# Kernel tuning notes

Hardware: AMD Instinct MI355X
Metric: run time of the kernel (lower is better)

## Reference

```python
import jax, jax.numpy as jnp
import numpy as np

N_NODES = 50000
N_EDGES = 800000
F_IN = 128
HIDDEN = 96
N_CLASS = 40


def setup_inputs() -> dict:
    key = jax.random.key(0)
    ks = jax.random.split(key, 16)
    x = jax.random.normal(ks[0], (N_NODES, F_IN), dtype=jnp.float32)
    edge_index = jax.random.randint(ks[1], (2, N_EDGES), 0, N_NODES, dtype=jnp.int64)
    edge_weight = jax.random.uniform(ks[2], (N_EDGES,), dtype=jnp.float32)
    s = 0.1
    return {
        "x": x,
        "edge_index": edge_index,
        "edge_weight": edge_weight,
        "W_conv1": jax.random.normal(ks[3], (F_IN, HIDDEN), dtype=jnp.float32) * s,
        "b_conv1": jnp.zeros((HIDDEN,), dtype=jnp.float32),
        "W_conv2": jax.random.normal(ks[4], (HIDDEN, HIDDEN), dtype=jnp.float32) * s,
        "b_conv2": jnp.zeros((HIDDEN,), dtype=jnp.float32),
        "W_conv3": jax.random.normal(ks[5], (HIDDEN, HIDDEN), dtype=jnp.float32) * s,
        "b_conv3": jnp.zeros((HIDDEN,), dtype=jnp.float32),
        "W_lin1": jax.random.normal(ks[6], (F_IN, HIDDEN), dtype=jnp.float32) * s,
        "b_lin1": jnp.zeros((HIDDEN,), dtype=jnp.float32),
        "W_lin2": jax.random.normal(ks[7], (HIDDEN, N_CLASS), dtype=jnp.float32) * s,
        "b_lin2": jnp.zeros((N_CLASS,), dtype=jnp.float32),
    }


def _gcn_norm(edge_index, edge_weight, num_nodes):
    # PyG gcn_norm: add self-loops (weight 1), symmetric deg^-1/2 normalization.
    row, col = edge_index[0], edge_index[1]
    loop = jnp.arange(num_nodes, dtype=edge_index.dtype)
    rows = jnp.concatenate([row, loop])
    cols = jnp.concatenate([col, loop])
    w = jnp.concatenate([edge_weight, jnp.ones((num_nodes,), edge_weight.dtype)])
    deg = jax.ops.segment_sum(w, cols, num_segments=num_nodes)
    dinv = jnp.where(deg > 0, jax.lax.rsqrt(deg), 0.0)
    norm = dinv[rows] * w * dinv[cols]  # [E + N]
    return rows, cols, norm


def _gcn_conv(x, rows, cols, norm, W, b, num_nodes):
    h = x @ W                                   # [N, H]
    msg = norm[:, None] * h[rows]               # gather + scale, [E+N, H]
    out = jax.ops.segment_sum(msg, cols, num_segments=num_nodes)  # scatter-add
    return out + b


def reference(x, edge_index, edge_weight, W_conv1, b_conv1, W_conv2, b_conv2,
              W_conv3, b_conv3, W_lin1, b_lin1, W_lin2, b_lin2):
    N = x.shape[0]
    rows, cols, norm = _gcn_norm(edge_index, edge_weight, N)
    # x1 = elu(conv1(x)); residual branch through first_lin + stacked convs
    x1 = jax.nn.elu(_gcn_conv(x, rows, cols, norm, W_conv1, b_conv1, N))
    h = jax.nn.elu(x @ W_lin1 + b_lin1)
    # dropout p=0.5 is identity in eval mode
    h = jax.nn.elu(_gcn_conv(h, rows, cols, norm, W_conv2, b_conv2, N))
    h = jax.nn.elu(_gcn_conv(h, rows, cols, norm, W_conv3, b_conv3, N))
    h = x1 + h
    logits = h @ W_lin2 + b_lin2
    return jax.nn.log_softmax(logits, axis=-1)
```

## Files before the change

### kernel.cpp

```cpp
#include <hip/hip_runtime.h>
#include <hip/hip_bf16.h>

static __device__ __forceinline__ float elu_f(float x) {
    return x > 0.f ? x : expm1f(x);
}

static __device__ __forceinline__ ushort f2bf(float x) {
    __hip_bfloat16 h = __float2bfloat16(x);
    ushort u;
    __builtin_memcpy(&u, &h, 2);
    return u;
}

typedef short bf16x8 __attribute__((ext_vector_type(8)));
typedef float f32x4  __attribute__((ext_vector_type(4)));
typedef float floatx2 __attribute__((ext_vector_type(2)));

#if __has_builtin(__builtin_amdgcn_cvt_pk_f32_fp8) && __has_builtin(__builtin_amdgcn_cvt_pk_fp8_f32)
#define FP8_HW 1
#else
#define FP8_HW 0
#endif

static __device__ __forceinline__ float fp8_to_f32_sw(uint b) {
    uint s = (b & 0x80u) << 24;
    uint e = (b >> 3) & 0xfu, m = b & 7u;
    float v = (e == 0) ? ((float)m * 0x1p-9f)
                       : __uint_as_float(((e + 120u) << 23) | (m << 20));
    return __uint_as_float(s | __float_as_uint(v));
}

static __device__ __forceinline__ uint f32_to_fp8_sw(float x) {
    float c = fminf(fmaxf(x, -448.f), 448.f);
    uint s = (__float_as_uint(c) >> 24) & 0x80u;
    float a = fabsf(c);
    uint bits;
    if (a < 0x1p-6f) {
        int mi = (int)rintf(a * 0x1p9f);
        bits = (mi >= 8) ? 0x08u : (uint)mi;
    } else {
        uint u = __float_as_uint(a);
        int eb = (int)((u >> 23) & 0xff) - 127;
        float sc = a * exp2f((float)(3 - eb));
        int q = (int)rintf(sc);
        if (q >= 16) { q = 8; eb += 1; }
        bits = (eb > 8) ? 0x7eu : (((uint)(eb + 7) << 3) | (uint)(q - 8));
    }
    return s | bits;
}

static __device__ __forceinline__ uchar f2fp8(float v) {
#if FP8_HW
    return (uchar)((uint)__builtin_amdgcn_cvt_pk_fp8_f32(v, v, 0, false) & 0xffu);
#else
    return (uchar)f32_to_fp8_sw(v);
#endif
}

static __device__ __forceinline__ void fp8x4_unpack(uint w, float* f) {
#if FP8_HW
    floatx2 p0 = __builtin_amdgcn_cvt_pk_f32_fp8((int)w, false);
    floatx2 p1 = __builtin_amdgcn_cvt_pk_f32_fp8((int)w, true);
    f[0] = p0[0]; f[1] = p0[1]; f[2] = p1[0]; f[3] = p1[1];
#else
    f[0] = fp8_to_f32_sw(w & 0xffu);
    f[1] = fp8_to_f32_sw((w >> 8) & 0xffu);
    f[2] = fp8_to_f32_sw((w >> 16) & 0xffu);
    f[3] = fp8_to_f32_sw(w >> 24);
#endif
}

static __device__ __forceinline__ void fp8x16_unpack(uint4 v, float* f) {
    fp8x4_unpack(v.x, f);
    fp8x4_unpack(v.y, f + 4);
    fp8x4_unpack(v.z, f + 8);
    fp8x4_unpack(v.w, f + 12);
}

static __device__ __forceinline__ void bf8_unpack(uint4 v, float* f) {
    f[0] = __uint_as_float(v.x << 16);
    f[1] = __uint_as_float(v.x & 0xffff0000u);
    f[2] = __uint_as_float(v.y << 16);
    f[3] = __uint_as_float(v.y & 0xffff0000u);
    f[4] = __uint_as_float(v.z << 16);
    f[5] = __uint_as_float(v.z & 0xffff0000u);
    f[6] = __uint_as_float(v.w << 16);
    f[7] = __uint_as_float(v.w & 0xffff0000u);
}

static __device__ __forceinline__ uint4 bf8_pack(const float* a) {
    uint4 o;
    o.x = (uint)f2bf(a[0]) | ((uint)f2bf(a[1]) << 16);
    o.y = (uint)f2bf(a[2]) | ((uint)f2bf(a[3]) << 16);
    o.z = (uint)f2bf(a[4]) | ((uint)f2bf(a[5]) << 16);
    o.w = (uint)f2bf(a[6]) | ((uint)f2bf(a[7]) << 16);
    return o;
}

__global__ __launch_bounds__(256) void
k_wprep_count(const float* __restrict__ W1, const float* __restrict__ W2,
              const float* __restrict__ W3, const float* __restrict__ W4,
              ushort* __restrict__ T1, ushort* __restrict__ T2,
              ushort* __restrict__ T3, ushort* __restrict__ T4,
              const int* __restrict__ col, int* __restrict__ bcnt,
              int E, int bspan, int nW) {
    const int b = blockIdx.x;
    if (b < nW) {
        const float* W; ushort* T; int K, base;
        if      (b < 48)  { W = W1; T = T1; K = 128; base = b;       }
        else if (b < 96)  { W = W2; T = T2; K = 128; base = b - 48;  }
        else if (b < 132) { W = W3; T = T3; K = 96;  base = b - 96;  }
        else              { W = W4; T = T4; K = 96;  base = b - 132; }
        const int i = base * 256 + threadIdx.x;
        const int kk = i / 96, c = i - kk * 96;
        T[c * K + kk] = f2bf(W[i]);
    } else {
        __shared__ int h[256];
        const int tid = threadIdx.x;
        h[tid] = 0;
        __syncthreads();
        const int e0 = (b - nW) * 4096;
        #pragma unroll
        for (int j = 0; j < 16; ++j) {
            int e = e0 + j * 256 + tid;
            if (e < E) atomicAdd(&h[col[e] / bspan], 1);
        }
        __syncthreads();
        if (h[tid] > 0) atomicAdd(&bcnt[tid], h[tid]);
    }
}

__global__ __launch_bounds__(256) void
k_bscatter(const int* __restrict__ row, const int* __restrict__ col,
           const float* __restrict__ w, const int* __restrict__ bcnt,
           int* __restrict__ bRes, int2* __restrict__ ebuf, int* __restrict__ edst,
           int E, int bspan) {
    __shared__ int h[256];
    __shared__ int base[256];
    __shared__ int sOff[256];
    __shared__ int wsum[4];
    const int tid = threadIdx.x, lane = tid & 63, wid = tid >> 6;
    h[tid] = 0;
    const int bc = bcnt[tid];
    __syncthreads();
    const int e0 = blockIdx.x * 4096;
    int bk[16], rk[16];
    #pragma unroll
    for (int j = 0; j < 16; ++j) {
        int e = e0 + j * 256 + tid;
        if (e < E) {
            int b = col[e] / bspan;
            bk[j] = b;
            rk[j] = atomicAdd(&h[b], 1);
        }
    }
    {
        int s = bc;
        #pragma unroll
        for (int d = 1; d < 64; d <<= 1) {
            int t = __shfl_up(s, d);
            if (lane >= d) s += t;
        }
        if (lane == 63) wsum[wid] = s;
        __syncthreads();
        int wb = 0;
        #pragma unroll
        for (int k = 0; k < 3; ++k) if (k < wid) wb += wsum[k];
        sOff[tid] = s - bc + wb;
    }
    __syncthreads();
    base[tid] = (h[tid] > 0) ? (sOff[tid] + atomicAdd(&bRes[tid], h[tid])) : 0;
    __syncthreads();
    #pragma unroll
    for (int j = 0; j < 16; ++j) {
        int e = e0 + j * 256 + tid;
        if (e < E) {
            int pos = base[bk[j]] + rk[j];
            ebuf[pos] = make_int2(row[e], __float_as_int(w[e]));
            edst[pos] = col[e];
        }
    }
}

__global__ __launch_bounds__(256) void
k_csrify(const int2* __restrict__ ebuf, const int* __restrict__ edst,
         const int* __restrict__ bcnt, int* __restrict__ off, float* __restrict__ dinv,
         int2* __restrict__ pairs, int N, int E, int bspan) {
    __shared__ int hist[256];
    __shared__ float degs[256];
    __shared__ int curl[256];
    __shared__ int wsum[4];
    __shared__ int sE0;
    const int tid = threadIdx.x, b = blockIdx.x;
    const int lane = tid & 63, wid = tid >> 6;
    const int base = b * bspan;
    const int lnodes = (N - base < bspan) ? (N - base) : bspan;
    if (b == 0 && tid == 0) off[N] = E;
    if (lnodes <= 0) return;
    hist[tid] = 0;
    degs[tid] = 0.f;
    const int bc = bcnt[tid];
    {
        int s = bc;
        #pragma unroll
        for (int d = 1; d < 64; d <<= 1) {
            int t = __shfl_up(s, d);
            if (lane >= d) s += t;
        }
        if (lane == 63) wsum[wid] = s;
        __syncthreads();
        int wb = 0;
        #pragma unroll
        for (int k = 0; k < 3; ++k) if (k < wid) wb += wsum[k];
        if (tid == b) sE0 = s - bc + wb;
    }
    __syncthreads();
    const int e0 = sE0, e1 = sE0 + bcnt[b];
    for (int e = e0 + tid; e < e1; e += 256) {
        int d = edst[e] - base;
        atomicAdd(&hist[d], 1);
        atomicAdd(&degs[d], __int_as_float(ebuf[e].y));
    }
    __syncthreads();
    int v = hist[tid];
    int s = v;
    #pragma unroll
    for (int d = 1; d < 64; d <<= 1) {
        int t = __shfl_up(s, d);
        if (lane >= d) s += t;
    }
    if (lane == 63) wsum[wid] = s;
    __syncthreads();
    int wb = 0;
    #pragma unroll
    for (int k = 0; k < 3; ++k) if (k < wid) wb += wsum[k];
    int excl = s - v + wb;
    if (tid < lnodes) {
        off[base + tid] = e0 + excl;
        dinv[base + tid] = rsqrtf(1.0f + degs[tid]);
    }
    curl[tid] = excl;
    __syncthreads();
    for (int e = e0 + tid; e < e1; e += 256) {
        int d = edst[e] - base;
        int p = atomicAdd(&curl[d], 1);
        pairs[e0 + p] = ebuf[e];
    }
}

template<int K, int XBF>
__device__ __forceinline__ void gemm_body(
    const void* __restrict__ Xv, const ushort* __restrict__ Wt,
    const float* __restrict__ bias, const float* __restrict__ dscale,
    void* __restrict__ outp, int N, int act, int ofp8, int bid) {
    constexpr int KP = K + 8;
    __shared__ ushort XT[64 * KP];
    __shared__ ushort WT[96 * KP];
    const int tid = threadIdx.x;
    const int n0  = bid * 64;

    #pragma unroll
    for (int i = tid; i < 96 * K / 8; i += 256) {
        const int c = i / (K / 8), q = i - c * (K / 8);
        uint4 v = reinterpret_cast<const uint4*>(Wt)[i];
        *reinterpret_cast<uint4*>(&WT[c * KP + q * 8]) = v;
    }
    if (XBF) {
        const ushort* X = (const ushort*)Xv;
        #pragma unroll
        for (int i = tid; i < 64 * K / 8; i += 256) {
            const int row = i / (K / 8), q = i - row * (K / 8);
            const int n = (n0 + row < N) ? (n0 + row) : (N - 1);
            uint4 v = *reinterpret_cast<const uint4*>(X + (size_t)n * K + q * 8);
            *reinterpret_cast<uint4*>(&XT[row * KP + q * 8]) = v;
        }
    } else {
        const float* X = (const float*)Xv;
        #pragma unroll
        for (int i = tid; i < 64 * K / 4; i += 256) {
            const int row = i / (K / 4), q = i - row * (K / 4);
            const int n = (n0 + row < N) ? (n0 + row) : (N - 1);
            float4 v = *reinterpret_cast<const float4*>(X + (size_t)n * K + q * 4);
            uint lo = (uint)f2bf(v.x) | ((uint)f2bf(v.y) << 16);
            uint hi = (uint)f2bf(v.z) | ((uint)f2bf(v.w) << 16);
            *reinterpret_cast<uint2*>(&XT[row * KP + q * 4]) = make_uint2(lo, hi);
        }
    }
    __syncthreads();

    const int lane = tid & 63;
    const int wv   = tid >> 6;
    const int r16  = lane & 15;
    const int kh   = lane >> 4;

    bf16x8 a[K / 32];
    const ushort* xbase = &XT[(wv * 16 + r16) * KP + kh * 8];
    #pragma unroll
    for (int ks = 0; ks < K / 32; ++ks)
        a[ks] = *reinterpret_cast<const bf16x8*>(xbase + ks * 32);

    f32x4 acc[6];
    #pragma unroll
    for (int ct = 0; ct < 6; ++ct) {
        f32x4 c = {0.f, 0.f, 0.f, 0.f};
        const ushort* wbase = &WT[(ct * 16 + r16) * KP + kh * 8];
        #pragma unroll
        for (int ks = 0; ks < K / 32; ++ks) {
            bf16x8 bfr = *reinterpret_cast<const bf16x8*>(wbase + ks * 32);
            c = __builtin_amdgcn_mfma_f32_16x16x32_bf16(a[ks], bfr, c, 0, 0, 0);
        }
        acc[ct] = c;
    }

    #pragma unroll
    for (int r = 0; r < 4; ++r) {
        const int n = n0 + wv * 16 + kh * 4 + r;
        if (n >= N) continue;
        const float ds = dscale ? dscale[n] : 1.f;
        #pragma unroll
        for (int ct = 0; ct < 6; ++ct) {
            const int col = ct * 16 + r16;
            float v = acc[ct][r] * ds;
            if (bias) v += bias[col];
            if (act) v = elu_f(v);
            if (ofp8) ((uchar*)outp)[(size_t)n * 96 + col] = f2fp8(v);
            else      ((ushort*)outp)[(size_t)n * 96 + col] = f2bf(v);
        }
    }
}

__global__ __launch_bounds__(256) void
k_gemm_mfma96(const ushort* __restrict__ X, const ushort* __restrict__ Wt,
              const float* __restrict__ dscale, void* __restrict__ outp, int N) {
    gemm_body<96, 1>(X, Wt, nullptr, dscale, outp, N, 0, 1, blockIdx.x);
}

__global__ __launch_bounds__(256) void
k_gemm_fin_dual(const float* __restrict__ X,
                const ushort* __restrict__ Wt1, const float* __restrict__ dscale1,
                void* __restrict__ out1,
                const ushort* __restrict__ Wt2, const float* __restrict__ bias2,
                void* __restrict__ out2, int N, int nHalf) {
    if ((int)blockIdx.x < nHalf)
        gemm_body<128, 0>(X, Wt1, nullptr, dscale1, out1, N, 0, 1, blockIdx.x);
    else
        gemm_body<128, 0>(X, Wt2, bias2, nullptr, out2, N, 1, 0, blockIdx.x - nHalf);
}

#define AGG_CAP 2048

__global__ __launch_bounds__(256) void
k_aggregate(const uchar* __restrict__ tmp, const int* __restrict__ off,
            const int2* __restrict__ pairs, const float* __restrict__ dinv,
            const float* __restrict__ bias, const ushort* __restrict__ addsrc,
            ushort* __restrict__ out, int N) {
    __shared__ int2 eP[AGG_CAP];
    __shared__ int sFlag;
    const int tid = threadIdx.x;
    const int t0  = blockIdx.x * 256;
    int n_first = t0 / 6;
    if (n_first >= N) return;
    int n_last = (t0 + 255) / 6;
    if (n_last >= N) n_last = N - 1;
    const int eb0 = off[n_first];
    const int eb1 = off[n_last + 1];
    const int tot = eb1 - eb0;
    if (tot <= AGG_CAP) {
        for (int i = tid; i < tot; i += 256) eP[i] = pairs[eb0 + i];
        if (tid == 0) sFlag = 1;
    } else if (tid == 0) sFlag = 0;
    __syncthreads();
    const bool lds = (sFlag != 0);

    const int n = (t0 + tid) / 6;
    if (n >= N) return;
    const int c = ((t0 + tid) % 6) * 16;
    const uchar* base = tmp + c;

    auto LOADP = [&](int e) -> int2 { return lds ? eP[e - eb0] : pairs[e]; };

    const float di = dinv[n];
    float f[16], acc[16];
    {
        uint4 sv = *reinterpret_cast<const uint4*>(base + (size_t)n * 96);
        fp8x16_unpack(sv, f);
        #pragma unroll
        for (int i = 0; i < 16; ++i) acc[i] = f[i];
    }

    const int e0 = off[n];
    const int e1 = off[n + 1];
    const int m  = e1 - e0;

    int2 pA, pB, pC;
    uint4 hA, hB, hC;
    if (m > 0) { pA = LOADP(e0);     hA = *reinterpret_cast<const uint4*>(base + (size_t)pA.x * 96); }
    if (m > 1) { pB = LOADP(e0 + 1); hB = *reinterpret_cast<const uint4*>(base + (size_t)pB.x * 96); }
    if (m > 2) { pC = LOADP(e0 + 2); hC = *reinterpret_cast<const uint4*>(base + (size_t)pC.x * 96); }

    for (int e = e0 + 3; e < e1; ++e) {
        int2 pD = LOADP(e);
        uint4 hD = *reinterpret_cast<const uint4*>(base + (size_t)pD.x * 96);
        float w = __int_as_float(pA.y);
        fp8x16_unpack(hA, f);
        #pragma unroll
        for (int i = 0; i < 16; ++i) acc[i] = fmaf(w, f[i], acc[i]);
        pA = pB; hA = hB;
        pB = pC; hB = hC;
        pC = pD; hC = hD;
    }
    if (m > 0) {
        float w = __int_as_float(pA.y);
        fp8x16_unpack(hA, f);
        #pragma unroll
        for (int i = 0; i < 16; ++i) acc[i] = fmaf(w, f[i], acc[i]);
    }
    if (m > 1) {
        float w = __int_as_float(pB.y);
        fp8x16_unpack(hB, f);
        #pragma unroll
        for (int i = 0; i < 16; ++i) acc[i] = fmaf(w, f[i], acc[i]);
    }
    if (m > 2) {
        float w = __int_as_float(pC.y);
        fp8x16_unpack(hC, f);
        #pragma unroll
        for (int i = 0; i < 16; ++i) acc[i] = fmaf(w, f[i], acc[i]);
    }

    #pragma unroll
    for (int q = 0; q < 4; ++q) {
        float4 bv = *reinterpret_cast<const float4*>(bias + c + q * 4);
        acc[q * 4 + 0] = elu_f(fmaf(di, acc[q * 4 + 0], bv.x));
        acc[q * 4 + 1] = elu_f(fmaf(di, acc[q * 4 + 1], bv.y));
        acc[q * 4 + 2] = elu_f(fmaf(di, acc[q * 4 + 2], bv.z));
        acc[q * 4 + 3] = elu_f(fmaf(di, acc[q * 4 + 3], bv.w));
    }
    if (addsrc) {
        uint4 r0 = *reinterpret_cast<const uint4*>(addsrc + (size_t)n * 96 + c);
        uint4 r1 = *reinterpret_cast<const uint4*>(addsrc + (size_t)n * 96 + c + 8);
        bf8_unpack(r0, f);
        bf8_unpack(r1, f + 8);
        #pragma unroll
        for (int i = 0; i < 16; ++i) acc[i] += f[i];
    }
    ushort* op = out + (size_t)n * 96 + c;
    *reinterpret_cast<uint4*>(op)     = bf8_pack(acc);
    *reinterpret_cast<uint4*>(op + 8) = bf8_pack(acc + 8);
}

__global__ __launch_bounds__(128) void
k_lin2_lsm(const ushort* __restrict__ h, const float* __restrict__ W2,
           const float* __restrict__ b2, float* __restrict__ out, int N) {
    __shared__ float hsT[96][128];
    const int tid = threadIdx.x;
    const int n0 = blockIdx.x * 128;
    const int nn = (N - n0 < 128) ? (N - n0) : 128;

    if (tid < nn) {
        const ushort* hr = h + (size_t)(n0 + tid) * 96;
        #pragma unroll
        for (int q = 0; q < 12; ++q) {
            uint4 v = *reinterpret_cast<const uint4*>(hr + q * 8);
            float f[8];
            bf8_unpack(v, f);
            #pragma unroll
            for (int j = 0; j < 8; ++j) hsT[q * 8 + j][tid] = f[j];
        }
    }
    __syncthreads();

    float acc[40];
    #pragma unroll
    for (int c = 0; c < 40; ++c) acc[c] = b2[c];
    for (int k = 0; k < 96; ++k) {
        const float hv = hsT[k][tid];
        const float* wr = W2 + k * 40;
        #pragma unroll
        for (int c = 0; c < 40; ++c) acc[c] = fmaf(hv, wr[c], acc[c]);
    }

    float m = acc[0];
    #pragma unroll
    for (int c = 1; c < 40; ++c) m = fmaxf(m, acc[c]);
    float s = 0.f;
    #pragma unroll
    for (int c = 0; c < 40; ++c) s += expf(acc[c] - m);
    const float lse = m + logf(s);

    if (tid < nn) {
        float* op = out + (size_t)(n0 + tid) * 40;
        #pragma unroll
        for (int q = 0; q < 10; ++q) {
            float4 v = make_float4(acc[q * 4 + 0] - lse, acc[q * 4 + 1] - lse,
                                   acc[q * 4 + 2] - lse, acc[q * 4 + 3] - lse);
            *reinterpret_cast<float4*>(op + q * 4) = v;
        }
    }
}


extern "C" void kernel_launch(void* const* d_in, const int* in_sizes, int n_in,
                              void* d_out, int out_size, void* d_ws, size_t ws_size,
                              hipStream_t stream) {
    const float* x   = (const float*)d_in[0];
    const int*   ei  = (const int*)d_in[1];
    const float* ew  = (const float*)d_in[2];
    const float* Wc1 = (const float*)d_in[3];
    const float* bc1 = (const float*)d_in[4];
    const float* Wc2 = (const float*)d_in[5];
    const float* bc2 = (const float*)d_in[6];
    const float* Wc3 = (const float*)d_in[7];
    const float* bc3 = (const float*)d_in[8];
    const float* Wl1 = (const float*)d_in[9];
    const float* bl1 = (const float*)d_in[10];
    const float* Wl2 = (const float*)d_in[11];
    const float* bl2 = (const float*)d_in[12];

    const int FIN = 128, HID = 96;
    const int N = in_sizes[0] / FIN;
    const int E = in_sizes[2];
    const int* row = ei;
    const int* col = ei + E;
    const int bspan = (N + 255) / 256;

    char* ws = (char*)d_ws;
    size_t o = 0;
    auto alloc = [&](size_t bytes) -> void* {
        void* p = ws + o;
        o += (bytes + 255) & ~(size_t)255;
        return p;
    };
    float*  dinv   = (float*)alloc((size_t)N * 4);
    int*    off    = (int*)  alloc((size_t)(N + 1) * 4);
    int*    bmem   = (int*)  alloc(512 * 4);
    int*    bcnt   = bmem;
    int*    bRes   = bmem + 256;
    int2*   pairs  = (int2*) alloc((size_t)E * 8);
    uchar*  M1     = (uchar*)alloc((size_t)N * HID);
    uchar*  M2     = (uchar*)alloc((size_t)N * HID);
    ushort* Bb     = (ushort*)alloc((size_t)N * HID * 2);
    ushort* Cb     = (ushort*)alloc((size_t)N * HID * 2);
    ushort* Wt_c1  = (ushort*)alloc(96 * 128 * 2);
    ushort* Wt_l1  = (ushort*)alloc(96 * 128 * 2);
    ushort* Wt_c2  = (ushort*)alloc(96 * 96 * 2);
    ushort* Wt_c3  = (ushort*)alloc(96 * 96 * 2);
    int2*   ebuf   = (int2*) alloc((size_t)E * 8);
    int*    edst   = (int*)  alloc((size_t)E * 4);

    const int gBkt  = (E + 4095) / 4096;
    const int nGemm = (N + 63) / 64;
    const int nAgg  = (N * 6 + 255) / 256;

    hipMemsetAsync(bmem, 0, 512 * 4, stream);
    k_wprep_count<<<168 + gBkt, 256, 0, stream>>>(Wc1, Wl1, Wc2, Wc3,
                                                  Wt_c1, Wt_l1, Wt_c2, Wt_c3,
                                                  col, bcnt, E, bspan, 168);

    k_bscatter<<<gBkt, 256, 0, stream>>>(row, col, ew, bcnt, bRes, ebuf, edst, E, bspan);
    k_csrify<<<256, 256, 0, stream>>>(ebuf, edst, bcnt, off, dinv, pairs, N, E, bspan);

    k_gemm_fin_dual<<<2 * nGemm, 256, 0, stream>>>(x, Wt_c1, dinv, M1,
                                                   Wt_l1, bl1, Cb, N, nGemm);

    k_aggregate<<<nAgg, 256, 0, stream>>>(M1, off, pairs, dinv, bc1, nullptr, Bb, N);

    k_gemm_mfma96<<<nGemm, 256, 0, stream>>>(Cb, Wt_c2, dinv, M2, N);
    k_aggregate<<<nAgg, 256, 0, stream>>>(M2, off, pairs, dinv, bc2, nullptr, Cb, N);

    k_gemm_mfma96<<<nGemm, 256, 0, stream>>>(Cb, Wt_c3, dinv, M1, N);
    k_aggregate<<<nAgg, 256, 0, stream>>>(M1, off, pairs, dinv, bc3, Bb, Cb, N);

    k_lin2_lsm<<<(N + 127) / 128, 128, 0, stream>>>(Cb, Wl2, bl2, (float*)d_out, N);
}
```

Baseline: 186.0 us.

## Fuse aggregation with next-layer GEMM and co-schedule independent stages

Runs the first aggregation and the conv2 GEMM in one launch, since the two are independent and can be split by block index. Fuses the second aggregation with the conv3 GEMM so aggregated rows stay in LDS as bf16 and feed MFMA directly, which avoids writing and re-reading the intermediate buffer. Also stores bf16 instead of float in the lin2 shared buffer to halve LDS use. This saves two launches and one global round trip, at the cost of a larger block with more LDS and lower occupancy in the fused kernel.

```diff
diff --git a/kernel.cpp b/kernel.cpp
--- a/kernel.cpp
+++ b/kernel.cpp
@@ -330,12 +330,6 @@
 }
 
 __global__ __launch_bounds__(256) void
-k_gemm_mfma96(const ushort* __restrict__ X, const ushort* __restrict__ Wt,
-              const float* __restrict__ dscale, void* __restrict__ outp, int N) {
-    gemm_body<96, 1>(X, Wt, nullptr, dscale, outp, N, 0, 1, blockIdx.x);
-}
-
-__global__ __launch_bounds__(256) void
 k_gemm_fin_dual(const float* __restrict__ X,
                 const ushort* __restrict__ Wt1, const float* __restrict__ dscale1,
                 void* __restrict__ out1,
@@ -349,15 +343,15 @@
 
 #define AGG_CAP 2048
 
-__global__ __launch_bounds__(256) void
-k_aggregate(const uchar* __restrict__ tmp, const int* __restrict__ off,
-            const int2* __restrict__ pairs, const float* __restrict__ dinv,
-            const float* __restrict__ bias, const ushort* __restrict__ addsrc,
-            ushort* __restrict__ out, int N) {
+__device__ __forceinline__ void agg_body(
+    const uchar* __restrict__ tmp, const int* __restrict__ off,
+    const int2* __restrict__ pairs, const float* __restrict__ dinv,
+    const float* __restrict__ bias, const ushort* __restrict__ addsrc,
+    ushort* __restrict__ out, int N, int bid) {
     __shared__ int2 eP[AGG_CAP];
     __shared__ int sFlag;
     const int tid = threadIdx.x;
-    const int t0  = blockIdx.x * 256;
+    const int t0  = bid * 256;
     int n_first = t0 / 6;
     if (n_first >= N) return;
     int n_last = (t0 + 255) / 6;
@@ -449,10 +443,160 @@
     *reinterpret_cast<uint4*>(op + 8) = bf8_pack(acc + 8);
 }
 
+__global__ __launch_bounds__(256) void
+k_aggregate(const uchar* __restrict__ tmp, const int* __restrict__ off,
+            const int2* __restrict__ pairs, const float* __restrict__ dinv,
+            const float* __restrict__ bias, const ushort* __restrict__ addsrc,
+            ushort* __restrict__ out, int N) {
+    agg_body(tmp, off, pairs, dinv, bias, addsrc, out, N, blockIdx.x);
+}
+
+__global__ __launch_bounds__(256) void
+k_agg1_gemm2(const uchar* __restrict__ M1, const int* __restrict__ off,
+             const int2* __restrict__ pairs, const float* __restrict__ dinv,
+             const float* __restrict__ bc1, ushort* __restrict__ Bb,
+             const ushort* __restrict__ Cb, const ushort* __restrict__ Wt2,
+             uchar* __restrict__ M2, int N, int nAgg) {
+    if ((int)blockIdx.x < nAgg)
+        agg_body(M1, off, pairs, dinv, bc1, nullptr, Bb, N, blockIdx.x);
+    else
+        gemm_body<96, 1>(Cb, Wt2, nullptr, dinv, M2, N, 0, 1, (int)blockIdx.x - nAgg);
+}
+
+#define FKP 104
+
+__global__ __launch_bounds__(384) void
+k_agg2_gemm3(const uchar* __restrict__ M2, const int* __restrict__ off,
+             const int2* __restrict__ pairs, const float* __restrict__ dinv,
+             const float* __restrict__ bc2, const ushort* __restrict__ Wt3,
+             uchar* __restrict__ M3, int N) {
+    __shared__ ushort XT[64 * FKP];
+    __shared__ ushort WT[96 * FKP];
+    __shared__ int2 eP[AGG_CAP];
+    __shared__ int sFlag;
+    const int tid = threadIdx.x;
+    const int n0  = blockIdx.x * 64;
+
+    for (int i = tid; i < 96 * 96 / 8; i += 384) {
+        const int c = i / 12, q = i - c * 12;
+        uint4 v = reinterpret_cast<const uint4*>(Wt3)[i];
+        *reinterpret_cast<uint4*>(&WT[c * FKP + q * 8]) = v;
+    }
+    int n_last = (n0 + 63 < N) ? (n0 + 63) : (N - 1);
+    const int eb0 = off[n0];
+    const int eb1 = off[n_last + 1];
+    const int tot = eb1 - eb0;
+    if (tot <= AGG_CAP) {
+        for (int i = tid; i < tot; i += 384) eP[i] = pairs[eb0 + i];
+        if (tid == 0) sFlag = 1;
+    } else if (tid == 0) sFlag = 0;
+    __syncthreads();
+    const bool lds = (sFlag != 0);
+
+    const int n = n0 + tid / 6;
+    const int c = (tid % 6) * 16;
+    float acc[16];
+    if (n < N) {
+        const uchar* base = M2 + c;
+        auto LOADP = [&](int e) -> int2 { return lds ? eP[e - eb0] : pairs[e]; };
+        float f[16];
+        {
+            uint4 sv = *reinterpret_cast<const uint4*>(base + (size_t)n * 96);
+            fp8x16_unpack(sv, f);
+            #pragma unroll
+            for (int i = 0; i < 16; ++i) acc[i] = f[i];
+        }
+        const int e0 = off[n];
+        const int e1 = off[n + 1];
+        const int m  = e1 - e0;
+        int2 pA, pB, pC;
+        uint4 hA, hB, hC;
+        if (m > 0) { pA = LOADP(e0);     hA = *reinterpret_cast<const uint4*>(base + (size_t)pA.x * 96); }
+        if (m > 1) { pB = LOADP(e0 + 1); hB = *reinterpret_cast<const uint4*>(base + (size_t)pB.x * 96); }
+        if (m > 2) { pC = LOADP(e0 + 2); hC = *reinterpret_cast<const uint4*>(base + (size_t)pC.x * 96); }
+        for (int e = e0 + 3; e < e1; ++e) {
+            int2 pD = LOADP(e);
+            uint4 hD = *reinterpret_cast<const uint4*>(base + (size_t)pD.x * 96);
+            float w = __int_as_float(pA.y);
+            fp8x16_unpack(hA, f);
+            #pragma unroll
+            for (int i = 0; i < 16; ++i) acc[i] = fmaf(w, f[i], acc[i]);
+            pA = pB; hA = hB;
+            pB = pC; hB = hC;
+            pC = pD; hC = hD;
+        }
+        if (m > 0) {
+            float w = __int_as_float(pA.y);
+            fp8x16_unpack(hA, f);
+            #pragma unroll
+            for (int i = 0; i < 16; ++i) acc[i] = fmaf(w, f[i], acc[i]);
+        }
+        if (m > 1) {
+            float w = __int_as_float(pB.y);
+            fp8x16_unpack(hB, f);
+            #pragma unroll
+            for (int i = 0; i < 16; ++i) acc[i] = fmaf(w, f[i], acc[i]);
+        }
+        if (m > 2) {
+            float w = __int_as_float(pC.y);
+            fp8x16_unpack(hC, f);
+            #pragma unroll
+            for (int i = 0; i < 16; ++i) acc[i] = fmaf(w, f[i], acc[i]);
+        }
+        const float di = dinv[n];
+        #pragma unroll
+        for (int q = 0; q < 4; ++q) {
+            float4 bv = *reinterpret_cast<const float4*>(bc2 + c + q * 4);
+            acc[q * 4 + 0] = elu_f(fmaf(di, acc[q * 4 + 0], bv.x));
+            acc[q * 4 + 1] = elu_f(fmaf(di, acc[q * 4 + 1], bv.y));
+            acc[q * 4 + 2] = elu_f(fmaf(di, acc[q * 4 + 2], bv.z));
+            acc[q * 4 + 3] = elu_f(fmaf(di, acc[q * 4 + 3], bv.w));
+        }
+    } else {
+        #pragma unroll
+        for (int i = 0; i < 16; ++i) acc[i] = 0.f;
+    }
+    {
+        ushort* xp = &XT[(tid / 6) * FKP + c];
+        *reinterpret_cast<uint4*>(xp)     = bf8_pack(acc);
+        *reinterpret_cast<uint4*>(xp + 8) = bf8_pack(acc + 8);
+    }
+    __syncthreads();
+
+    const int lane = tid & 63;
+    const int ct   = tid >> 6;
+    const int r16  = lane & 15;
+    const int kh   = lane >> 4;
+
+    bf16x8 b[3];
+    const ushort* wbase = &WT[(ct * 16 + r16) * FKP + kh * 8];
+    #pragma unroll
+    for (int ks = 0; ks < 3; ++ks)
+        b[ks] = *reinterpret_cast<const bf16x8*>(wbase + ks * 32);
+
+    #pragma unroll
+    for (int rt = 0; rt < 4; ++rt) {
+        f32x4 d = {0.f, 0.f, 0.f, 0.f};
+        const ushort* xb = &XT[(rt * 16 + r16) * FKP + kh * 8];
+        #pragma unroll
+        for (int ks = 0; ks < 3; ++ks) {
+            bf16x8 a = *reinterpret_cast<const bf16x8*>(xb + ks * 32);
+            d = __builtin_amdgcn_mfma_f32_16x16x32_bf16(a, b[ks], d, 0, 0, 0);
+        }
+        const int col = ct * 16 + r16;
+        #pragma unroll
+        for (int r = 0; r < 4; ++r) {
+            const int nrow = n0 + rt * 16 + kh * 4 + r;
+            if (nrow < N)
+                M3[(size_t)nrow * 96 + col] = f2fp8(d[r] * dinv[nrow]);
+        }
+    }
+}
+
 __global__ __launch_bounds__(128) void
 k_lin2_lsm(const ushort* __restrict__ h, const float* __restrict__ W2,
            const float* __restrict__ b2, float* __restrict__ out, int N) {
-    __shared__ float hsT[96][128];
+    __shared__ ushort hsT[96][128];
     const int tid = threadIdx.x;
     const int n0 = blockIdx.x * 128;
     const int nn = (N - n0 < 128) ? (N - n0) : 128;
@@ -462,10 +606,14 @@
         #pragma unroll
         for (int q = 0; q < 12; ++q) {
             uint4 v = *reinterpret_cast<const uint4*>(hr + q * 8);
-            float f[8];
-            bf8_unpack(v, f);
-            #pragma unroll
-            for (int j = 0; j < 8; ++j) hsT[q * 8 + j][tid] = f[j];
+            hsT[q * 8 + 0][tid] = (ushort)(v.x & 0xffffu);
+            hsT[q * 8 + 1][tid] = (ushort)(v.x >> 16);
+            hsT[q * 8 + 2][tid] = (ushort)(v.y & 0xffffu);
+            hsT[q * 8 + 3][tid] = (ushort)(v.y >> 16);
+            hsT[q * 8 + 4][tid] = (ushort)(v.z & 0xffffu);
+            hsT[q * 8 + 5][tid] = (ushort)(v.z >> 16);
+            hsT[q * 8 + 6][tid] = (ushort)(v.w & 0xffffu);
+            hsT[q * 8 + 7][tid] = (ushort)(v.w >> 16);
         }
     }
     __syncthreads();
@@ -474,7 +622,7 @@
     #pragma unroll
     for (int c = 0; c < 40; ++c) acc[c] = b2[c];
     for (int k = 0; k < 96; ++k) {
-        const float hv = hsT[k][tid];
+        const float hv = __uint_as_float((uint)hsT[k][tid] << 16);
         const float* wr = W2 + k * 40;
         #pragma unroll
         for (int c = 0; c < 40; ++c) acc[c] = fmaf(hv, wr[c], acc[c]);
@@ -539,6 +687,7 @@
     int2*   pairs  = (int2*) alloc((size_t)E * 8);
     uchar*  M1     = (uchar*)alloc((size_t)N * HID);
     uchar*  M2     = (uchar*)alloc((size_t)N * HID);
+    uchar*  M3     = (uchar*)alloc((size_t)N * HID);
     ushort* Bb     = (ushort*)alloc((size_t)N * HID * 2);
     ushort* Cb     = (ushort*)alloc((size_t)N * HID * 2);
     ushort* Wt_c1  = (ushort*)alloc(96 * 128 * 2);
@@ -563,13 +712,12 @@
     k_gemm_fin_dual<<<2 * nGemm, 256, 0, stream>>>(x, Wt_c1, dinv, M1,
                                                    Wt_l1, bl1, Cb, N, nGemm);
 
-    k_aggregate<<<nAgg, 256, 0, stream>>>(M1, off, pairs, dinv, bc1, nullptr, Bb, N);
-
-    k_gemm_mfma96<<<nGemm, 256, 0, stream>>>(Cb, Wt_c2, dinv, M2, N);
-    k_aggregate<<<nAgg, 256, 0, stream>>>(M2, off, pairs, dinv, bc2, nullptr, Cb, N);
-
-    k_gemm_mfma96<<<nGemm, 256, 0, stream>>>(Cb, Wt_c3, dinv, M1, N);
-    k_aggregate<<<nAgg, 256, 0, stream>>>(M1, off, pairs, dinv, bc3, Bb, Cb, N);
+    k_agg1_gemm2<<<nAgg + nGemm, 256, 0, stream>>>(M1, off, pairs, dinv, bc1, Bb,
+                                                   Cb, Wt_c2, M2, N, nAgg);
+
+    k_agg2_gemm3<<<nGemm, 384, 0, stream>>>(M2, off, pairs, dinv, bc2, Wt_c3, M3, N);
+
+    k_aggregate<<<nAgg, 256, 0, stream>>>(M3, off, pairs, dinv, bc3, Bb, Cb, N);
 
     k_lin2_lsm<<<(N + 127) / 128, 128, 0, stream>>>(Cb, Wl2, bl2, (float*)d_out, N);
 }
```

Result: slower. 197.4 us (+6.1%).

## Co-launch conv1 aggregation with independent conv2 GEMM; store bf16 in lin2 LDS

Applied to the files above, without the earlier changes.

Layer-1 aggregation and the conv2 GEMM (which depends only on the lin1 output Cb) are independent, so they now run as one launch with a block-index split. This removes a kernel launch and the serialization between them, letting both share the GPU. A separate M3 buffer is added for the conv3 GEMM output, and the lin2/log-softmax kernel keeps bf16 values in LDS instead of fp32, halving shared memory per block at the cost of a shift per read. The fused kernel's register and LDS footprint becomes the maximum of the two bodies, which may lower occupancy.

```diff
diff --git a/kernel.cpp b/kernel.cpp
--- a/kernel.cpp
+++ b/kernel.cpp
@@ -349,15 +349,15 @@
 
 #define AGG_CAP 2048
 
-__global__ __launch_bounds__(256) void
-k_aggregate(const uchar* __restrict__ tmp, const int* __restrict__ off,
-            const int2* __restrict__ pairs, const float* __restrict__ dinv,
-            const float* __restrict__ bias, const ushort* __restrict__ addsrc,
-            ushort* __restrict__ out, int N) {
+__device__ __forceinline__ void agg_body(
+    const uchar* __restrict__ tmp, const int* __restrict__ off,
+    const int2* __restrict__ pairs, const float* __restrict__ dinv,
+    const float* __restrict__ bias, const ushort* __restrict__ addsrc,
+    ushort* __restrict__ out, int N, int bid) {
     __shared__ int2 eP[AGG_CAP];
     __shared__ int sFlag;
     const int tid = threadIdx.x;
-    const int t0  = blockIdx.x * 256;
+    const int t0  = bid * 256;
     int n_first = t0 / 6;
     if (n_first >= N) return;
     int n_last = (t0 + 255) / 6;
@@ -449,10 +449,30 @@
     *reinterpret_cast<uint4*>(op + 8) = bf8_pack(acc + 8);
 }
 
+__global__ __launch_bounds__(256) void
+k_aggregate(const uchar* __restrict__ tmp, const int* __restrict__ off,
+            const int2* __restrict__ pairs, const float* __restrict__ dinv,
+            const float* __restrict__ bias, const ushort* __restrict__ addsrc,
+            ushort* __restrict__ out, int N) {
+    agg_body(tmp, off, pairs, dinv, bias, addsrc, out, N, blockIdx.x);
+}
+
+__global__ __launch_bounds__(256) void
+k_agg1_gemm2(const uchar* __restrict__ M1, const int* __restrict__ off,
+             const int2* __restrict__ pairs, const float* __restrict__ dinv,
+             const float* __restrict__ bc1, ushort* __restrict__ Bb,
+             const ushort* __restrict__ Cb, const ushort* __restrict__ Wt2,
+             uchar* __restrict__ M2, int N, int nAgg) {
+    if ((int)blockIdx.x < nAgg)
+        agg_body(M1, off, pairs, dinv, bc1, nullptr, Bb, N, blockIdx.x);
+    else
+        gemm_body<96, 1>(Cb, Wt2, nullptr, dinv, M2, N, 0, 1, (int)blockIdx.x - nAgg);
+}
+
 __global__ __launch_bounds__(128) void
 k_lin2_lsm(const ushort* __restrict__ h, const float* __restrict__ W2,
            const float* __restrict__ b2, float* __restrict__ out, int N) {
-    __shared__ float hsT[96][128];
+    __shared__ ushort hsT[96][128];
     const int tid = threadIdx.x;
     const int n0 = blockIdx.x * 128;
     const int nn = (N - n0 < 128) ? (N - n0) : 128;
@@ -462,10 +482,14 @@
         #pragma unroll
         for (int q = 0; q < 12; ++q) {
             uint4 v = *reinterpret_cast<const uint4*>(hr + q * 8);
-            float f[8];
-            bf8_unpack(v, f);
-            #pragma unroll
-            for (int j = 0; j < 8; ++j) hsT[q * 8 + j][tid] = f[j];
+            hsT[q * 8 + 0][tid] = (ushort)(v.x & 0xffffu);
+            hsT[q * 8 + 1][tid] = (ushort)(v.x >> 16);
+            hsT[q * 8 + 2][tid] = (ushort)(v.y & 0xffffu);
+            hsT[q * 8 + 3][tid] = (ushort)(v.y >> 16);
+            hsT[q * 8 + 4][tid] = (ushort)(v.z & 0xffffu);
+            hsT[q * 8 + 5][tid] = (ushort)(v.z >> 16);
+            hsT[q * 8 + 6][tid] = (ushort)(v.w & 0xffffu);
+            hsT[q * 8 + 7][tid] = (ushort)(v.w >> 16);
         }
     }
     __syncthreads();
@@ -474,7 +498,7 @@
     #pragma unroll
     for (int c = 0; c < 40; ++c) acc[c] = b2[c];
     for (int k = 0; k < 96; ++k) {
-        const float hv = hsT[k][tid];
+        const float hv = __uint_as_float((uint)hsT[k][tid] << 16);
         const float* wr = W2 + k * 40;
         #pragma unroll
         for (int c = 0; c < 40; ++c) acc[c] = fmaf(hv, wr[c], acc[c]);
@@ -539,6 +563,7 @@
     int2*   pairs  = (int2*) alloc((size_t)E * 8);
     uchar*  M1     = (uchar*)alloc((size_t)N * HID);
     uchar*  M2     = (uchar*)alloc((size_t)N * HID);
+    uchar*  M3     = (uchar*)alloc((size_t)N * HID);
     ushort* Bb     = (ushort*)alloc((size_t)N * HID * 2);
     ushort* Cb     = (ushort*)alloc((size_t)N * HID * 2);
     ushort* Wt_c1  = (ushort*)alloc(96 * 128 * 2);
@@ -563,13 +588,14 @@
     k_gemm_fin_dual<<<2 * nGemm, 256, 0, stream>>>(x, Wt_c1, dinv, M1,
                                                    Wt_l1, bl1, Cb, N, nGemm);
 
-    k_aggregate<<<nAgg, 256, 0, stream>>>(M1, off, pairs, dinv, bc1, nullptr, Bb, N);
-
-    k_gemm_mfma96<<<nGemm, 256, 0, stream>>>(Cb, Wt_c2, dinv, M2, N);
+    k_agg1_gemm2<<<nAgg + nGemm, 256, 0, stream>>>(M1, off, pairs, dinv, bc1, Bb,
+                                                   Cb, Wt_c2, M2, N, nAgg);
+
     k_aggregate<<<nAgg, 256, 0, stream>>>(M2, off, pairs, dinv, bc2, nullptr, Cb, N);
 
-    k_gemm_mfma96<<<nGemm, 256, 0, stream>>>(Cb, Wt_c3, dinv, M1, N);
-    k_aggregate<<<nAgg, 256, 0, stream>>>(M1, off, pairs, dinv, bc3, Bb, Cb, N);
+    k_gemm_mfma96<<<nGemm, 256, 0, stream>>>(Cb, Wt_c3, dinv, M3, N);
+
+    k_aggregate<<<nAgg, 256, 0, stream>>>(M3, off, pairs, dinv, bc3, Bb, Cb, N);
 
     k_lin2_lsm<<<(N + 127) / 128, 128, 0, stream>>>(Cb, Wl2, bl2, (float*)d_out, N);
 }
```

Measured after the change: 187.8 us. No clear change (+1.0%).
